# Kernel optimization log

Hardware: AMD Instinct MI355X
Metric: run time of the kernel (lower is better)

Reference implementation:

```python
import jax, jax.numpy as jnp
import numpy as np
from jax import lax

# LNS semantics: values are held as (sign, log_base|x|); exact conversion round-trips
# make log-domain mul/add mathematically identical to float conv/linear/relu, so the
# faithful reference is the equivalent float pipeline.

def _conv(x, w, b):
    # x: [B,C,H,W], w: [O,C,kh,kw] (torch layout), stride 1, no padding
    y = lax.conv_general_dilated(x, w, window_strides=(1, 1), padding='VALID',
                                 dimension_numbers=('NCHW', 'OIHW', 'NCHW'))
    return y + b[None, :, None, None]

def _maxpool2(x):
    return lax.reduce_window(x, -jnp.inf, lax.max,
                             window_dimensions=(1, 1, 2, 2),
                             window_strides=(1, 1, 2, 2), padding='VALID')

def setup_inputs() -> dict:
    key = jax.random.key(0)
    ks = jax.random.split(key, 9)
    s = lambda k, shape, fan: jax.random.normal(k, shape, jnp.float32) * (1.0 / np.sqrt(fan))
    return {
        'x': jax.random.normal(ks[0], (512, 1, 54, 54), jnp.float32),
        'conv1_w': s(ks[1], (32, 1, 3, 3), 9),
        'conv1_b': s(ks[2], (32,), 9),
        'conv2_w': s(ks[3], (64, 32, 3, 3), 32 * 9),
        'conv2_b': s(ks[4], (64,), 32 * 9),
        'fc1_w': s(ks[5], (128, 9216), 9216),
        'fc1_b': s(ks[6], (128,), 9216),
        'fc2_w': s(ks[7], (10, 128), 128),
        'fc2_b': s(ks[8], (10,), 128),
    }

def reference(x, conv1_w, conv1_b, conv2_w, conv2_b, fc1_w, fc1_b, fc2_w, fc2_b):
    h = jnp.maximum(_conv(x, conv1_w, conv1_b), 0.0)          # [B,32,52,52]
    h = _maxpool2(h)                                          # [B,32,26,26]
    h = jnp.maximum(_conv(h, conv2_w, conv2_b), 0.0)          # [B,64,24,24]
    h = _maxpool2(h)                                          # [B,64,12,12]
    h = h.reshape(h.shape[0], -1)                             # [B,9216]
    h = jnp.maximum(h @ fc1_w.T + fc1_b, 0.0)                 # [B,128]
    return h @ fc2_w.T + fc2_b                                # [B,10]
```

## Files before the change

kernel.cpp:

```cpp
#include <hip/hip_runtime.h>


#define B 512
#define POS 676
#define ICP 36
#define P2SZ (64*12*12)
#define SCR 26
#define IMS 58
#define IMCOPY (54 * IMS)

typedef unsigned short ushort_t;
typedef ushort_t ushort4v __attribute__((ext_vector_type(4)));
typedef _Float16 f16x8 __attribute__((ext_vector_type(8)));
typedef float f32x4 __attribute__((ext_vector_type(4)));

__device__ __forceinline__ ushort_t f2h(float f) {
    union { _Float16 h; ushort_t u; } a; a.h = (_Float16)f; return a.u;
}
__device__ __forceinline__ float h2f(ushort_t u) {
    union { ushort_t u; _Float16 h; } a; a.u = u; return (float)a.h;
}

#define N_WR (64 * 9 * 32)
#define CONV1_BLOCKS 1024
#define WR_BLOCKS 72
#define TR_BLOCKS 128

__global__ __launch_bounds__(256) void conv1_prep(const float* __restrict__ x,
                                                  const float* __restrict__ w,
                                                  const float* __restrict__ bias,
                                                  const float* __restrict__ c2w,
                                                  const float* __restrict__ f1w,
                                                  ushort_t* __restrict__ out,
                                                  ushort_t* __restrict__ wr,
                                                  ushort_t* __restrict__ wfb) {
    __shared__ char smem[64 * 145 * 4];
    int blk = blockIdx.x;
    int tid = threadIdx.x;

    if (blk >= CONV1_BLOCKS + WR_BLOCKS) {
        float* tr = reinterpret_cast<float*>(smem);
        int n = blk - CONV1_BLOCKS - WR_BLOCKS;
        const float* src = f1w + (size_t)n * 9216;
#pragma unroll
        for (int i = 0; i < 36; ++i) {
            int idx = i * 256 + tid;
            int oc = idx / 144, pos = idx - oc * 144;
            tr[oc * 145 + pos] = src[idx];
        }
        __syncthreads();
        ushort_t* dst = wfb + (size_t)n * 9216;
#pragma unroll
        for (int i = 0; i < 36; ++i) {
            int idx = i * 256 + tid;
            int pos = idx >> 6, oc = idx & 63;
            dst[idx] = f2h(tr[oc * 145 + pos]);
        }
        return;
    }
    if (blk >= CONV1_BLOCKS) {
        int t = (blk - CONV1_BLOCKS) * 256 + tid;
        int ic  = t & 31;
        int tap = (t >> 5) % 9;
        int oc  = t / 288;
        wr[t] = f2h(c2w[oc * 288 + ic * 9 + tap]);
        return;
    }

    ushort_t* lds = reinterpret_cast<ushort_t*>(smem);
    int b    = blk >> 1;
    int half = blk & 1;

    for (int i = tid; i < 54; i += 256) {
        ushort_t* r0 = lds + i * IMS;
        r0[54] = 0; r0[55] = 0; r0[56] = 0; r0[57] = 0;
        ushort_t* r1 = lds + IMCOPY + i * IMS;
        r1[53] = 0; r1[54] = 0; r1[55] = 0; r1[56] = 0; r1[57] = 0;
    }
    if (tid < 64) lds[2 * IMCOPY + tid] = 0;

    const float* xim = x + (size_t)b * 2916;
    for (int i = tid; i < 2916; i += 256) {
        int r = i / 54, c = i - r * 54;
        ushort_t v = f2h(xim[i]);
        lds[r * IMS + c] = v;
        if (c > 0) lds[IMCOPY + r * IMS + c - 1] = v;
    }

    int lane = tid & 63, wid = tid >> 6;
    int quad = lane >> 4, lr = lane & 15;

    f16x8 bfrag[2];
#pragma unroll
    for (int n = 0; n < 2; ++n) {
        union { ushort_t u[8]; f16x8 v; } bu;
#pragma unroll
        for (int j = 0; j < 8; ++j) bu.u[j] = 0;
        if (quad < 3) {
            const float* wp = w + (n * 16 + lr) * 9 + quad * 3;
            bu.u[0] = f2h(wp[0]);
            bu.u[1] = f2h(wp[1]);
            bu.u[2] = f2h(wp[2]);
        }
        bfrag[n] = bu.v;
    }
    float bv0 = bias[lr], bv1 = bias[16 + lr];

    __syncthreads();

    int cbase = (lr & 1) ? (IMCOPY + lr - 1) : lr;

    for (int py_l = wid; py_l < 13; py_l += 4) {
        int py = half * 13 + py_l;
        int y0 = 2 * py;
#pragma unroll
        for (int t = 0; t < 4; ++t) {
            int x0 = t * 16;
            int off0 = cbase + x0 + (y0 + quad) * IMS;
            int off1 = off0 + IMS;
            union { unsigned d[4]; f16x8 v; } a0, a1;
            a0.d[0] = *reinterpret_cast<const unsigned*>(&lds[off0]);
            a0.d[1] = *reinterpret_cast<const unsigned*>(&lds[off0 + 2]);
            a0.d[2] = a0.d[0]; a0.d[3] = a0.d[1];
            a1.d[0] = *reinterpret_cast<const unsigned*>(&lds[off1]);
            a1.d[1] = *reinterpret_cast<const unsigned*>(&lds[off1 + 2]);
            a1.d[2] = a1.d[0]; a1.d[3] = a1.d[1];

            f32x4 cA0 = (f32x4){0.f,0.f,0.f,0.f}, cA1 = cA0, cB0 = cA0, cB1 = cA0;
            cA0 = __builtin_amdgcn_mfma_f32_16x16x32_f16(a0.v, bfrag[0], cA0, 0, 0, 0);
            cA1 = __builtin_amdgcn_mfma_f32_16x16x32_f16(a0.v, bfrag[1], cA1, 0, 0, 0);
            cB0 = __builtin_amdgcn_mfma_f32_16x16x32_f16(a1.v, bfrag[0], cB0, 0, 0, 0);
            cB1 = __builtin_amdgcn_mfma_f32_16x16x32_f16(a1.v, bfrag[1], cB1, 0, 0, 0);

            if (t < 3 || quad == 0) {
                int px0 = t * 8 + quad * 2;
                float u0 = fmaxf(fmaxf(cA0[0], cA0[1]), fmaxf(cB0[0], cB0[1]));
                float u1 = fmaxf(fmaxf(cA0[2], cA0[3]), fmaxf(cB0[2], cB0[3]));
                float v0 = fmaxf(fmaxf(cA1[0], cA1[1]), fmaxf(cB1[0], cB1[1]));
                float v1 = fmaxf(fmaxf(cA1[2], cA1[3]), fmaxf(cB1[2], cB1[3]));
                ushort_t* po = out + ((size_t)b * POS + py * 26 + px0) * 32;
                po[lr]           = f2h(fmaxf(u0 + bv0, 0.0f));
                po[32 + lr]      = f2h(fmaxf(u1 + bv0, 0.0f));
                po[16 + lr]      = f2h(fmaxf(v0 + bv1, 0.0f));
                po[32 + 16 + lr] = f2h(fmaxf(v1 + bv1, 0.0f));
            }
        }
    }
}

__global__ __launch_bounds__(512) void conv2_mfma(const ushort_t* __restrict__ p1,
                                                  const ushort_t* __restrict__ wr,
                                                  const float* __restrict__ bias,
                                                  ushort_t* __restrict__ pool2cl) {
    __shared__ ushort_t lds[260 * ICP];
    int blk = blockIdx.x;
    int b = blk / 3, c = blk % 3;
    int tid = threadIdx.x;

    const ushort_t* src = p1 + ((size_t)b * POS + 8 * c * 26) * 32;
    for (int t = tid; t < 260 * 8; t += 512) {
        int pos = t >> 3, off = (t & 7) * 4;
        ushort4v v = *reinterpret_cast<const ushort4v*>(src + pos * 32 + off);
        *reinterpret_cast<ushort4v*>(&lds[pos * ICP + off]) = v;
    }
    __syncthreads();

    int lane = tid & 63, wid = tid >> 6;
    int quad = lane >> 4, lr = lane & 15;
    int prow = wid >> 1;
    int nhalf = wid & 1;

    int ebase[3];
#pragma unroll
    for (int t = 0; t < 3; ++t) {
        int m  = t * 16 + lr;
        int yl = m / 24;
        int xx = m - yl * 24;
        ebase[t] = ((2 * prow + yl) * 26 + xx) * ICP + quad * 8;
    }

    f32x4 acc[3][2];
#pragma unroll
    for (int t = 0; t < 3; ++t)
#pragma unroll
        for (int n = 0; n < 2; ++n) acc[t][n] = (f32x4){0.f, 0.f, 0.f, 0.f};

    const ushort_t* wb = wr + (size_t)(nhalf * 32 + lr) * 288 + quad * 8;

#pragma unroll
    for (int tap = 0; tap < 9; ++tap) {
        int ky = tap / 3, kx = tap % 3;
        int koff = (ky * 26 + kx) * ICP;
        f16x8 a[3];
#pragma unroll
        for (int t = 0; t < 3; ++t) {
            union { ushort4v s[2]; f16x8 v; } u;
            u.s[0] = *reinterpret_cast<const ushort4v*>(&lds[ebase[t] + koff]);
            u.s[1] = *reinterpret_cast<const ushort4v*>(&lds[ebase[t] + koff + 4]);
            a[t] = u.v;
        }
        f16x8 bf[2];
#pragma unroll
        for (int n = 0; n < 2; ++n)
            bf[n] = *reinterpret_cast<const f16x8*>(wb + (size_t)n * 16 * 288 + tap * 32);
#pragma unroll
        for (int t = 0; t < 3; ++t)
#pragma unroll
            for (int n = 0; n < 2; ++n)
                acc[t][n] = __builtin_amdgcn_mfma_f32_16x16x32_f16(a[t], bf[n], acc[t][n], 0, 0, 0);
    }
    __syncthreads();

    ushort_t* scr = lds + wid * (32 * SCR);
#pragma unroll
    for (int t = 0; t < 3; ++t)
#pragma unroll
        for (int n = 0; n < 2; ++n) {
            int ocl = n * 16 + lr;
            int i0 = t * 8 + quad * 2;
            float v0 = fmaxf(acc[t][n][0], acc[t][n][1]);
            float v1 = fmaxf(acc[t][n][2], acc[t][n][3]);
            union { ushort_t u2[2]; unsigned w; } pk;
            pk.u2[0] = f2h(v0); pk.u2[1] = f2h(v1);
            *reinterpret_cast<unsigned*>(&scr[ocl * SCR + i0]) = pk.w;
        }
    int ocl = lane & 31;
    int pxh = lane >> 5;
    int oc  = nhalf * 32 + ocl;
    const ushort_t* row = scr + ocl * SCR;
    float bv = bias[oc];
    int py = c * 4 + prow;
    ushort_t* po = pool2cl + ((size_t)b * 144 + py * 12) * 64 + oc;
#pragma unroll
    for (int j = 0; j < 6; ++j) {
        int px = pxh * 6 + j;
        float r0 = h2f(row[px]);
        float r1 = h2f(row[px + 12]);
        po[px * 64] = f2h(fmaxf(fmaxf(r0, r1) + bv, 0.0f));
    }
}

__global__ __launch_bounds__(256) void fc1_mfma(const ushort_t* __restrict__ A,
                                                 const ushort_t* __restrict__ W,
                                                 float* __restrict__ Cpart) {
    int tid = threadIdx.x;
    int lane = tid & 63, wid = tid >> 6;
    int lr = lane & 15, quad = lane >> 4;
    int w  = blockIdx.x * 4 + wid;
    int nt = w & 3;
    int ks = (w >> 2) & 15;
    int mt = w >> 6;

    int m0 = mt * 16;
    int n0 = nt * 32;
    int k0 = ks * 576 + quad * 8;
    const ushort_t* a0 = A + (size_t)(m0 + lr) * 9216 + k0;
    const ushort_t* b0 = W + (size_t)(n0 + lr) * 9216 + k0;
    const ushort_t* b1 = b0 + (size_t)16 * 9216;

    f32x4 acc0 = (f32x4){0.f, 0.f, 0.f, 0.f};
    f32x4 acc1 = (f32x4){0.f, 0.f, 0.f, 0.f};

#pragma unroll
    for (int kk = 0; kk < 18; ++kk) {
        f16x8 av  = *reinterpret_cast<const f16x8*>(a0 + kk * 32);
        f16x8 bv0 = *reinterpret_cast<const f16x8*>(b0 + kk * 32);
        f16x8 bv1 = *reinterpret_cast<const f16x8*>(b1 + kk * 32);
        acc0 = __builtin_amdgcn_mfma_f32_16x16x32_f16(av, bv0, acc0, 0, 0, 0);
        acc1 = __builtin_amdgcn_mfma_f32_16x16x32_f16(av, bv1, acc1, 0, 0, 0);
    }

    float* cp = Cpart + (size_t)ks * (512 * 128);
    int crow = m0 + quad * 4;
#pragma unroll
    for (int r = 0; r < 4; ++r) {
        cp[(size_t)(crow + r) * 128 + n0 + lr]      = acc0[r];
        cp[(size_t)(crow + r) * 128 + n0 + 16 + lr] = acc1[r];
    }
}

__global__ __launch_bounds__(256) void fc1fc2(const float* __restrict__ Cpart,
                                              const float* __restrict__ b1,
                                              const float* __restrict__ w2,
                                              const float* __restrict__ b2,
                                              float* __restrict__ out) {
    __shared__ float h[2][128];
    int half = threadIdx.x >> 7;
    int k = threadIdx.x & 127;
    int b = blockIdx.x * 2 + half;
    float s = 0.f;
#pragma unroll
    for (int ks = 0; ks < 16; ++ks) s += Cpart[(size_t)ks * (512 * 128) + b * 128 + k];
    h[half][k] = fmaxf(s + b1[k], 0.0f);
    __syncthreads();
    if (k < 10) {
        const float* wp = w2 + k * 128;
        float acc = 0.f;
#pragma unroll 8
        for (int j = 0; j < 128; ++j) acc += h[half][j] * wp[j];
        out[b * 10 + k] = acc + b2[k];
    }
}

extern "C" void kernel_launch(void* const* d_in, const int* in_sizes, int n_in,
                              void* d_out, int out_size, void* d_ws, size_t ws_size,
                              hipStream_t stream) {
    const float* x       = (const float*)d_in[0];
    const float* conv1_w = (const float*)d_in[1];
    const float* conv1_b = (const float*)d_in[2];
    const float* conv2_w = (const float*)d_in[3];
    const float* conv2_b = (const float*)d_in[4];
    const float* fc1_w   = (const float*)d_in[5];
    const float* fc1_b   = (const float*)d_in[6];
    const float* fc2_w   = (const float*)d_in[7];
    const float* fc2_b   = (const float*)d_in[8];
    float* out = (float*)d_out;

    char* ws = (char*)d_ws;
    ushort_t* pool1 = (ushort_t*)ws;
    ws += (size_t)B * POS * 32 * sizeof(ushort_t);
    ushort_t* wr = (ushort_t*)ws;
    ws += N_WR * sizeof(ushort_t) + 128;
    ushort_t* wfb = (ushort_t*)ws;
    ws += (size_t)128 * 9216 * sizeof(ushort_t) + 128;
    ushort_t* pool2cl = (ushort_t*)ws;
    ws += (size_t)B * P2SZ * sizeof(ushort_t) + 128;
    float* Cpart = (float*)ws;
    ws += (size_t)16 * 512 * 128 * sizeof(float) + 128;

    conv1_prep<<<CONV1_BLOCKS + WR_BLOCKS + TR_BLOCKS, 256, 0, stream>>>(
        x, conv1_w, conv1_b, conv2_w, fc1_w, pool1, wr, wfb);
    conv2_mfma<<<B * 3, 512, 0, stream>>>(pool1, wr, conv2_b, pool2cl);
    fc1_mfma<<<512, 256, 0, stream>>>(pool2cl, wfb, Cpart);
    fc1fc2<<<256, 256, 0, stream>>>(Cpart, fc1_b, fc2_w, fc2_b, out);
}
```

Baseline: 126.6 us.

## Fuse conv1 and conv2 into one per-image kernel keeping pool1 in LDS

Merges the conv1+pool and conv2+pool stages into a single kernel with one 512-thread block per image. The pooled conv1 activations stay in shared memory instead of being written to and read back from a global workspace buffer. The conv2 stage loops over three row chunks, and its scratch area reuses the LDS space that held the input image. Weight reformatting moves to its own small prep launch. The trade-off is a large per-block LDS footprint (about 62KB), which limits blocks per CU, and a much coarser grid of 512 blocks.

```diff
diff --git a/kernel.cpp b/kernel.cpp
--- a/kernel.cpp
+++ b/kernel.cpp
@@ -8,6 +8,8 @@
 #define SCR 26
 #define IMS 58
 #define IMCOPY (54 * IMS)
+#define PL_USH (POS * ICP)
+#define SCRATCH_USH 6656
 
 typedef unsigned short ushort_t;
 typedef ushort_t ushort4v __attribute__((ext_vector_type(4)));
@@ -22,73 +24,73 @@
 }
 
 #define N_WR (64 * 9 * 32)
-#define CONV1_BLOCKS 1024
 #define WR_BLOCKS 72
 #define TR_BLOCKS 128
 
-__global__ __launch_bounds__(256) void conv1_prep(const float* __restrict__ x,
-                                                  const float* __restrict__ w,
-                                                  const float* __restrict__ bias,
-                                                  const float* __restrict__ c2w,
-                                                  const float* __restrict__ f1w,
-                                                  ushort_t* __restrict__ out,
-                                                  ushort_t* __restrict__ wr,
-                                                  ushort_t* __restrict__ wfb) {
-    __shared__ char smem[64 * 145 * 4];
+__global__ __launch_bounds__(256) void prep(const float* __restrict__ c2w,
+                                            const float* __restrict__ f1w,
+                                            ushort_t* __restrict__ wr,
+                                            ushort_t* __restrict__ wfb) {
+    __shared__ float tr[64 * 145];
     int blk = blockIdx.x;
     int tid = threadIdx.x;
 
-    if (blk >= CONV1_BLOCKS + WR_BLOCKS) {
-        float* tr = reinterpret_cast<float*>(smem);
-        int n = blk - CONV1_BLOCKS - WR_BLOCKS;
-        const float* src = f1w + (size_t)n * 9216;
-#pragma unroll
-        for (int i = 0; i < 36; ++i) {
-            int idx = i * 256 + tid;
-            int oc = idx / 144, pos = idx - oc * 144;
-            tr[oc * 145 + pos] = src[idx];
-        }
-        __syncthreads();
-        ushort_t* dst = wfb + (size_t)n * 9216;
-#pragma unroll
-        for (int i = 0; i < 36; ++i) {
-            int idx = i * 256 + tid;
-            int pos = idx >> 6, oc = idx & 63;
-            dst[idx] = f2h(tr[oc * 145 + pos]);
-        }
-        return;
-    }
-    if (blk >= CONV1_BLOCKS) {
-        int t = (blk - CONV1_BLOCKS) * 256 + tid;
+    if (blk < WR_BLOCKS) {
+        int t = blk * 256 + tid;
         int ic  = t & 31;
         int tap = (t >> 5) % 9;
         int oc  = t / 288;
         wr[t] = f2h(c2w[oc * 288 + ic * 9 + tap]);
         return;
     }
-
-    ushort_t* lds = reinterpret_cast<ushort_t*>(smem);
-    int b    = blk >> 1;
-    int half = blk & 1;
-
-    for (int i = tid; i < 54; i += 256) {
-        ushort_t* r0 = lds + i * IMS;
+    int n = blk - WR_BLOCKS;
+    const float* src = f1w + (size_t)n * 9216;
+#pragma unroll
+    for (int i = 0; i < 36; ++i) {
+        int idx = i * 256 + tid;
+        int oc = idx / 144, pos = idx - oc * 144;
+        tr[oc * 145 + pos] = src[idx];
+    }
+    __syncthreads();
+    ushort_t* dst = wfb + (size_t)n * 9216;
+#pragma unroll
+    for (int i = 0; i < 36; ++i) {
+        int idx = i * 256 + tid;
+        int pos = idx >> 6, oc = idx & 63;
+        dst[idx] = f2h(tr[oc * 145 + pos]);
+    }
+}
+
+__global__ __launch_bounds__(512, 4) void conv12(const float* __restrict__ x,
+                                                 const float* __restrict__ w1,
+                                                 const float* __restrict__ bias1,
+                                                 const ushort_t* __restrict__ wr,
+                                                 const float* __restrict__ bias2,
+                                                 ushort_t* __restrict__ pool2cl) {
+    __shared__ ushort_t smem[PL_USH + SCRATCH_USH];
+    ushort_t* pl  = smem;
+    ushort_t* img = smem + PL_USH;
+
+    int b   = blockIdx.x;
+    int tid = threadIdx.x;
+    int lane = tid & 63, wid = tid >> 6;
+    int quad = lane >> 4, lr = lane & 15;
+
+    for (int i = tid; i < 54; i += 512) {
+        ushort_t* r0 = img + i * IMS;
         r0[54] = 0; r0[55] = 0; r0[56] = 0; r0[57] = 0;
-        ushort_t* r1 = lds + IMCOPY + i * IMS;
+        ushort_t* r1 = img + IMCOPY + i * IMS;
         r1[53] = 0; r1[54] = 0; r1[55] = 0; r1[56] = 0; r1[57] = 0;
     }
-    if (tid < 64) lds[2 * IMCOPY + tid] = 0;
+    if (tid < 96) img[2 * IMCOPY + tid] = 0;
 
     const float* xim = x + (size_t)b * 2916;
-    for (int i = tid; i < 2916; i += 256) {
+    for (int i = tid; i < 2916; i += 512) {
         int r = i / 54, c = i - r * 54;
         ushort_t v = f2h(xim[i]);
-        lds[r * IMS + c] = v;
-        if (c > 0) lds[IMCOPY + r * IMS + c - 1] = v;
-    }
-
-    int lane = tid & 63, wid = tid >> 6;
-    int quad = lane >> 4, lr = lane & 15;
+        img[r * IMS + c] = v;
+        if (c > 0) img[IMCOPY + r * IMS + c - 1] = v;
+    }
 
     f16x8 bfrag[2];
 #pragma unroll
@@ -97,21 +99,22 @@
 #pragma unroll
         for (int j = 0; j < 8; ++j) bu.u[j] = 0;
         if (quad < 3) {
-            const float* wp = w + (n * 16 + lr) * 9 + quad * 3;
+            const float* wp = w1 + (n * 16 + lr) * 9 + quad * 3;
             bu.u[0] = f2h(wp[0]);
             bu.u[1] = f2h(wp[1]);
             bu.u[2] = f2h(wp[2]);
         }
         bfrag[n] = bu.v;
     }
-    float bv0 = bias[lr], bv1 = bias[16 + lr];
+    float bv0 = bias1[lr], bv1 = bias1[16 + lr];
 
     __syncthreads();
 
     int cbase = (lr & 1) ? (IMCOPY + lr - 1) : lr;
 
-    for (int py_l = wid; py_l < 13; py_l += 4) {
-        int py = half * 13 + py_l;
+    for (int it = 0; it < 4; ++it) {
+        int py = wid + it * 8;
+        if (py >= 26) break;
         int y0 = 2 * py;
 #pragma unroll
         for (int t = 0; t < 4; ++t) {
@@ -119,11 +122,11 @@
             int off0 = cbase + x0 + (y0 + quad) * IMS;
             int off1 = off0 + IMS;
             union { unsigned d[4]; f16x8 v; } a0, a1;
-            a0.d[0] = *reinterpret_cast<const unsigned*>(&lds[off0]);
-            a0.d[1] = *reinterpret_cast<const unsigned*>(&lds[off0 + 2]);
+            a0.d[0] = *reinterpret_cast<const unsigned*>(&img[off0]);
+            a0.d[1] = *reinterpret_cast<const unsigned*>(&img[off0 + 2]);
             a0.d[2] = a0.d[0]; a0.d[3] = a0.d[1];
-            a1.d[0] = *reinterpret_cast<const unsigned*>(&lds[off1]);
-            a1.d[1] = *reinterpret_cast<const unsigned*>(&lds[off1 + 2]);
+            a1.d[0] = *reinterpret_cast<const unsigned*>(&img[off1]);
+            a1.d[1] = *reinterpret_cast<const unsigned*>(&img[off1 + 2]);
             a1.d[2] = a1.d[0]; a1.d[3] = a1.d[1];
 
             f32x4 cA0 = (f32x4){0.f,0.f,0.f,0.f}, cA1 = cA0, cB0 = cA0, cB1 = cA0;
@@ -138,105 +141,90 @@
                 float u1 = fmaxf(fmaxf(cA0[2], cA0[3]), fmaxf(cB0[2], cB0[3]));
                 float v0 = fmaxf(fmaxf(cA1[0], cA1[1]), fmaxf(cB1[0], cB1[1]));
                 float v1 = fmaxf(fmaxf(cA1[2], cA1[3]), fmaxf(cB1[2], cB1[3]));
-                ushort_t* po = out + ((size_t)b * POS + py * 26 + px0) * 32;
-                po[lr]           = f2h(fmaxf(u0 + bv0, 0.0f));
-                po[32 + lr]      = f2h(fmaxf(u1 + bv0, 0.0f));
-                po[16 + lr]      = f2h(fmaxf(v0 + bv1, 0.0f));
-                po[32 + 16 + lr] = f2h(fmaxf(v1 + bv1, 0.0f));
+                ushort_t* po = pl + (py * 26 + px0) * ICP;
+                po[lr]            = f2h(fmaxf(u0 + bv0, 0.0f));
+                po[16 + lr]       = f2h(fmaxf(v0 + bv1, 0.0f));
+                po[ICP + lr]      = f2h(fmaxf(u1 + bv0, 0.0f));
+                po[ICP + 16 + lr] = f2h(fmaxf(v1 + bv1, 0.0f));
             }
         }
     }
-}
-
-__global__ __launch_bounds__(512) void conv2_mfma(const ushort_t* __restrict__ p1,
-                                                  const ushort_t* __restrict__ wr,
-                                                  const float* __restrict__ bias,
-                                                  ushort_t* __restrict__ pool2cl) {
-    __shared__ ushort_t lds[260 * ICP];
-    int blk = blockIdx.x;
-    int b = blk / 3, c = blk % 3;
-    int tid = threadIdx.x;
-
-    const ushort_t* src = p1 + ((size_t)b * POS + 8 * c * 26) * 32;
-    for (int t = tid; t < 260 * 8; t += 512) {
-        int pos = t >> 3, off = (t & 7) * 4;
-        ushort4v v = *reinterpret_cast<const ushort4v*>(src + pos * 32 + off);
-        *reinterpret_cast<ushort4v*>(&lds[pos * ICP + off]) = v;
-    }
+
     __syncthreads();
 
-    int lane = tid & 63, wid = tid >> 6;
-    int quad = lane >> 4, lr = lane & 15;
-    int prow = wid >> 1;
+    int prow  = wid >> 1;
     int nhalf = wid & 1;
-
-    int ebase[3];
-#pragma unroll
-    for (int t = 0; t < 3; ++t) {
-        int m  = t * 16 + lr;
-        int yl = m / 24;
-        int xx = m - yl * 24;
-        ebase[t] = ((2 * prow + yl) * 26 + xx) * ICP + quad * 8;
-    }
-
-    f32x4 acc[3][2];
-#pragma unroll
-    for (int t = 0; t < 3; ++t)
-#pragma unroll
-        for (int n = 0; n < 2; ++n) acc[t][n] = (f32x4){0.f, 0.f, 0.f, 0.f};
-
     const ushort_t* wb = wr + (size_t)(nhalf * 32 + lr) * 288 + quad * 8;
 
-#pragma unroll
-    for (int tap = 0; tap < 9; ++tap) {
-        int ky = tap / 3, kx = tap % 3;
-        int koff = (ky * 26 + kx) * ICP;
-        f16x8 a[3];
-#pragma unroll
-        for (int t = 0; t < 3; ++t) {
-            union { ushort4v s[2]; f16x8 v; } u;
-            u.s[0] = *reinterpret_cast<const ushort4v*>(&lds[ebase[t] + koff]);
-            u.s[1] = *reinterpret_cast<const ushort4v*>(&lds[ebase[t] + koff + 4]);
-            a[t] = u.v;
-        }
-        f16x8 bf[2];
-#pragma unroll
-        for (int n = 0; n < 2; ++n)
-            bf[n] = *reinterpret_cast<const f16x8*>(wb + (size_t)n * 16 * 288 + tap * 32);
-#pragma unroll
-        for (int t = 0; t < 3; ++t)
-#pragma unroll
-            for (int n = 0; n < 2; ++n)
-                acc[t][n] = __builtin_amdgcn_mfma_f32_16x16x32_f16(a[t], bf[n], acc[t][n], 0, 0, 0);
-    }
-    __syncthreads();
-
-    ushort_t* scr = lds + wid * (32 * SCR);
-#pragma unroll
-    for (int t = 0; t < 3; ++t)
-#pragma unroll
-        for (int n = 0; n < 2; ++n) {
-            int ocl = n * 16 + lr;
-            int i0 = t * 8 + quad * 2;
-            float v0 = fmaxf(acc[t][n][0], acc[t][n][1]);
-            float v1 = fmaxf(acc[t][n][2], acc[t][n][3]);
-            union { ushort_t u2[2]; unsigned w; } pk;
-            pk.u2[0] = f2h(v0); pk.u2[1] = f2h(v1);
-            *reinterpret_cast<unsigned*>(&scr[ocl * SCR + i0]) = pk.w;
-        }
     int ocl = lane & 31;
     int pxh = lane >> 5;
     int oc  = nhalf * 32 + ocl;
-    const ushort_t* row = scr + ocl * SCR;
-    float bv = bias[oc];
-    int py = c * 4 + prow;
-    ushort_t* po = pool2cl + ((size_t)b * 144 + py * 12) * 64 + oc;
-#pragma unroll
-    for (int j = 0; j < 6; ++j) {
-        int px = pxh * 6 + j;
-        float r0 = h2f(row[px]);
-        float r1 = h2f(row[px + 12]);
-        po[px * 64] = f2h(fmaxf(fmaxf(r0, r1) + bv, 0.0f));
+    float bv = bias2[oc];
+    ushort_t* scr = smem + PL_USH + wid * (32 * SCR);
+
+    for (int cc = 0; cc < 3; ++cc) {
+        int ebase[3];
+#pragma unroll
+        for (int t = 0; t < 3; ++t) {
+            int m  = t * 16 + lr;
+            int yl = m / 24;
+            int xx = m - yl * 24;
+            ebase[t] = ((8 * cc + 2 * prow + yl) * 26 + xx) * ICP + quad * 8;
+        }
+
+        f32x4 acc[3][2];
+#pragma unroll
+        for (int t = 0; t < 3; ++t)
+#pragma unroll
+            for (int n = 0; n < 2; ++n) acc[t][n] = (f32x4){0.f, 0.f, 0.f, 0.f};
+
+#pragma unroll
+        for (int tap = 0; tap < 9; ++tap) {
+            int ky = tap / 3, kx = tap % 3;
+            int koff = (ky * 26 + kx) * ICP;
+            f16x8 a[3];
+#pragma unroll
+            for (int t = 0; t < 3; ++t) {
+                union { ushort4v s[2]; f16x8 v; } u;
+                u.s[0] = *reinterpret_cast<const ushort4v*>(&pl[ebase[t] + koff]);
+                u.s[1] = *reinterpret_cast<const ushort4v*>(&pl[ebase[t] + koff + 4]);
+                a[t] = u.v;
+            }
+            f16x8 bf[2];
+#pragma unroll
+            for (int n = 0; n < 2; ++n)
+                bf[n] = *reinterpret_cast<const f16x8*>(wb + (size_t)n * 16 * 288 + tap * 32);
+#pragma unroll
+            for (int t = 0; t < 3; ++t)
+#pragma unroll
+                for (int n = 0; n < 2; ++n)
+                    acc[t][n] = __builtin_amdgcn_mfma_f32_16x16x32_f16(a[t], bf[n], acc[t][n], 0, 0, 0);
+        }
+
+#pragma unroll
+        for (int t = 0; t < 3; ++t)
+#pragma unroll
+            for (int n = 0; n < 2; ++n) {
+                int wocl = n * 16 + lr;
+                int i0 = t * 8 + quad * 2;
+                float v0 = fmaxf(acc[t][n][0], acc[t][n][1]);
+                float v1 = fmaxf(acc[t][n][2], acc[t][n][3]);
+                union { ushort_t u2[2]; unsigned w; } pk;
+                pk.u2[0] = f2h(v0); pk.u2[1] = f2h(v1);
+                *reinterpret_cast<unsigned*>(&scr[wocl * SCR + i0]) = pk.w;
+            }
+        __syncthreads();
+
+        const ushort_t* row = scr + ocl * SCR;
+        int py = cc * 4 + prow;
+        ushort_t* po = pool2cl + ((size_t)b * 144 + py * 12) * 64 + oc;
+#pragma unroll
+        for (int j = 0; j < 6; ++j) {
+            int px = pxh * 6 + j;
+            float r0 = h2f(row[px]);
+            float r1 = h2f(row[px + 12]);
+            po[px * 64] = f2h(fmaxf(fmaxf(r0, r1) + bv, 0.0f));
+        }
     }
 }
 
@@ -317,8 +305,6 @@
     float* out = (float*)d_out;
 
     char* ws = (char*)d_ws;
-    ushort_t* pool1 = (ushort_t*)ws;
-    ws += (size_t)B * POS * 32 * sizeof(ushort_t);
     ushort_t* wr = (ushort_t*)ws;
     ws += N_WR * sizeof(ushort_t) + 128;
     ushort_t* wfb = (ushort_t*)ws;
@@ -328,9 +314,8 @@
     float* Cpart = (float*)ws;
     ws += (size_t)16 * 512 * 128 * sizeof(float) + 128;
 
-    conv1_prep<<<CONV1_BLOCKS + WR_BLOCKS + TR_BLOCKS, 256, 0, stream>>>(
-        x, conv1_w, conv1_b, conv2_w, fc1_w, pool1, wr, wfb);
-    conv2_mfma<<<B * 3, 512, 0, stream>>>(pool1, wr, conv2_b, pool2cl);
+    prep<<<WR_BLOCKS + TR_BLOCKS, 256, 0, stream>>>(conv2_w, fc1_w, wr, wfb);
+    conv12<<<B, 512, 0, stream>>>(x, conv1_w, conv1_b, wr, conv2_b, pool2cl);
     fc1_mfma<<<512, 256, 0, stream>>>(pool2cl, wfb, Cpart);
     fc1fc2<<<256, 256, 0, stream>>>(Cpart, fc1_b, fc2_w, fc2_b, out);
 }
```

After: 119.3 us. 5.7% less time.
